# Kernel tuning notes

Hardware: AMD Instinct MI355X
Metric: run time of the kernel (lower is better)

## Reference

```python
import jax, jax.numpy as jnp
import numpy as np

B, C, H, W = 2, 192, 64, 64
HEADS, KS = 6, 7
HD = C // HEADS


def setup_inputs() -> dict:
    key = jax.random.key(0)
    ks = jax.random.split(key, 6)
    s = 0.02
    return {
        "x": jax.random.normal(ks[0], (B, C, H, W), jnp.float32),
        "W_qkv1": jax.random.normal(ks[1], (3 * C, C, 1, 1), jnp.float32) * s,
        "b_qkv1": jnp.zeros((3 * C,), jnp.float32),
        "W_qkv2": jax.random.normal(ks[2], (3 * C, 1, 3, 3), jnp.float32) * s,  # depthwise
        "b_qkv2": jnp.zeros((3 * C,), jnp.float32),
        "temperature": jnp.ones((HEADS, 1, 1, 1), jnp.float32),
        "rpb": jax.random.normal(ks[3], (HEADS, 2 * KS - 1, 2 * KS - 1), jnp.float32) * s,
        "W_proj": jax.random.normal(ks[4], (C, C, 1, 1), jnp.float32) * s,
        "b_proj": jnp.zeros((C,), jnp.float32),
    }


def _conv(x, w, b, pad, groups=1):
    y = jax.lax.conv_general_dilated(
        x, w, (1, 1), pad,
        dimension_numbers=("NCHW", "OIHW", "NCHW"),
        feature_group_count=groups)
    return y + b[None, :, None, None]


def _l2norm(t, eps=1e-12):
    n = jnp.sqrt(jnp.sum(t * t, axis=-1, keepdims=True))
    return t / jnp.maximum(n, eps)


def _nbr_idx(L, K):
    # NATTEN shifted-window neighborhood (dilation=1): window start clamped to image.
    start = jnp.clip(jnp.arange(L) - K // 2, 0, L - K)
    idx = start[:, None] + jnp.arange(K)[None, :]        # [L,K] absolute neighbor index
    rel = idx - jnp.arange(L)[:, None] + (K - 1)         # [L,K] rpb table index
    return idx, rel


def _forward(x, W_qkv1, b_qkv1, W_qkv2, b_qkv2, temperature, rpb, W_proj, b_proj):
    Bq, Cq, Hh, Ww = x.shape
    heads = rpb.shape[0]
    K = (rpb.shape[1] + 1) // 2
    hd = Cq // heads
    qkv = _conv(_conv(x, W_qkv1, b_qkv1, "VALID"), W_qkv2, b_qkv2, "SAME", groups=3 * Cq)
    qkv = qkv.reshape(Bq, 3, heads, hd, Hh, Ww).transpose(1, 0, 2, 4, 5, 3)  # [3,B,h,H,W,d]
    q, k, v = qkv[0], qkv[1], qkv[2]
    q = _l2norm(q)
    k = _l2norm(k)
    idx_i, rel_i = _nbr_idx(Hh, K)
    idx_j, rel_j = _nbr_idx(Ww, K)
    ii = idx_i[:, None, :, None]  # [H,1,K,1]
    jj = idx_j[None, :, None, :]  # [1,W,1,K] -> broadcast [H,W,K,K]
    k_nb = k[:, :, ii, jj, :]     # [B,h,H,W,K,K,d]
    attn = jnp.einsum("bhijd,bhijkld->bhijkl", q, k_nb)
    bias = rpb[:, rel_i[:, None, :, None], rel_j[None, :, None, :]]  # [h,H,W,K,K]
    attn = (attn + bias[None]) * temperature.reshape(1, heads, 1, 1, 1, 1)
    attn = jax.nn.softmax(attn.reshape(Bq, heads, Hh, Ww, K * K), axis=-1)
    v_nb = v[:, :, ii, jj, :].reshape(Bq, heads, Hh, Ww, K * K, hd)
    out = jnp.einsum("bhijk,bhijkd->bhijd", attn, v_nb)
    out = out.transpose(0, 1, 4, 2, 3).reshape(Bq, Cq, Hh, Ww)
    return _conv(out, W_proj, b_proj, "VALID")


def reference(x, W_qkv1, b_qkv1, W_qkv2, b_qkv2, temperature, rpb, W_proj, b_proj):
    return _forward(x, W_qkv1, b_qkv1, W_qkv2, b_qkv2, temperature, rpb, W_proj, b_proj)
```

## Files before the change

### kernel.cpp

```cpp
#include <hip/hip_runtime.h>
#include <math.h>

#define HW 4096

typedef __attribute__((ext_vector_type(8))) short short8;
typedef __attribute__((ext_vector_type(4))) float floatx4;

__device__ inline float bflo(unsigned u) { return __uint_as_float(u << 16); }
__device__ inline float bfhi(unsigned u) { return __uint_as_float(u & 0xffff0000u); }
__device__ inline unsigned short f2bf(float x) {
    unsigned u = __float_as_uint(x);
    return (unsigned short)((u + 0x7fffu + ((u >> 16) & 1u)) >> 16);
}
__device__ inline unsigned f2bf2(float lo, float hi) {
    unsigned a = __float_as_uint(lo), b = __float_as_uint(hi);
    a = (a + 0x7fffu + ((a >> 16) & 1u)) >> 16;
    b = (b + 0x7fffu + ((b >> 16) & 1u)) & 0xffff0000u;
    return a | b;
}
__device__ inline float qred(float x) {
    x += __int_as_float(__builtin_amdgcn_update_dpp(0, __float_as_int(x), 0xB1, 0xF, 0xF, true));
    x += __int_as_float(__builtin_amdgcn_update_dpp(0, __float_as_int(x), 0x4E, 0xF, 0xF, true));
    return x;
}


__global__ __launch_bounds__(256) void k_cvt(const float* __restrict__ W1,
    const float* __restrict__ Wp, unsigned short* __restrict__ Wb1,
    unsigned short* __restrict__ Wbp)
{
    int idx = blockIdx.x * 256 + threadIdx.x;
    if (idx < 110592) Wb1[idx] = f2bf(W1[idx]);
    else if (idx < 147456) Wbp[idx - 110592] = f2bf(Wp[idx - 110592]);
}

__global__ __launch_bounds__(256) void k_xt(const float* __restrict__ x,
    unsigned short* __restrict__ xT)
{
    __shared__ __align__(16) unsigned short tsm[64 * 196];
    const int t = threadIdx.x;
    const int px0 = blockIdx.x << 6;
    const int b = blockIdx.y;
    const float* xb = x + ((size_t)b * 192 << 12);
    #pragma unroll
    for (int pass = 0; pass < 12; ++pass) {
        int c = pass * 16 + (t >> 4);
        int p4 = t & 15;
        float4 v = *(const float4*)&xb[((size_t)c << 12) + px0 + p4 * 4];
        tsm[(p4 * 4 + 0) * 196 + c] = f2bf(v.x);
        tsm[(p4 * 4 + 1) * 196 + c] = f2bf(v.y);
        tsm[(p4 * 4 + 2) * 196 + c] = f2bf(v.z);
        tsm[(p4 * 4 + 3) * 196 + c] = f2bf(v.w);
    }
    __syncthreads();
    #pragma unroll
    for (int pass = 0; pass < 6; ++pass) {
        int idx = pass * 256 + t;
        int m = idx / 24, c8 = idx % 24;
        uint2 lo = *(const uint2*)&tsm[m * 196 + c8 * 8];
        uint2 hi = *(const uint2*)&tsm[m * 196 + c8 * 8 + 4];
        uint4 o = make_uint4(lo.x, lo.y, hi.x, hi.y);
        *(uint4*)&xT[((size_t)(b << 12) + px0 + m) * 192 + c8 * 8] = o;
    }
}

__global__ __launch_bounds__(256) void k_gq(const unsigned short* __restrict__ xT,
    const unsigned short* __restrict__ Wb1, const float* __restrict__ b1,
    unsigned short* __restrict__ qkv)
{
    __shared__ __align__(16) unsigned short As[64 * 200];
    __shared__ __align__(16) unsigned short Bs[64 * 200];
    const int t = threadIdx.x;
    const int m0 = blockIdx.x * 64;
    const int n0 = blockIdx.y * 64;
    #pragma unroll
    for (int pass = 0; pass < 6; ++pass) {
        int idx = pass * 256 + t;
        int m = idx / 24, c16 = idx % 24;
        *(uint4*)&As[m * 200 + c16 * 8] = *(const uint4*)&xT[(size_t)(m0 + m) * 192 + c16 * 8];
        *(uint4*)&Bs[m * 200 + c16 * 8] = *(const uint4*)&Wb1[(size_t)(n0 + m) * 192 + c16 * 8];
    }
    __syncthreads();
    const int w = t >> 6, lane = t & 63;
    const int lm = lane & 15, lq = lane >> 4;
    floatx4 acc[4] = {};
    #pragma unroll
    for (int ks = 0; ks < 6; ++ks) {
        short8 bf = *(const short8*)&Bs[(w * 16 + lm) * 200 + ks * 32 + lq * 8];
        #pragma unroll
        for (int mt = 0; mt < 4; ++mt) {
            short8 af = *(const short8*)&As[(mt * 16 + lm) * 200 + ks * 32 + lq * 8];
            acc[mt] = __builtin_amdgcn_mfma_f32_16x16x32_bf16(af, bf, acc[mt], 0, 0, 0);
        }
    }
    __syncthreads();
    const float bias = b1[n0 + w * 16 + lm];
    #pragma unroll
    for (int mt = 0; mt < 4; ++mt)
        #pragma unroll
        for (int r = 0; r < 4; ++r)
            As[(mt * 16 + lq * 4 + r) * 72 + w * 16 + lm] = f2bf(acc[mt][r] + bias);
    __syncthreads();
    #pragma unroll
    for (int pass = 0; pass < 2; ++pass) {
        int idx = pass * 256 + t;
        int m = idx >> 3, n8 = idx & 7;
        uint4 val = *(const uint4*)&As[m * 72 + n8 * 8];
        int mg = m0 + m;
        int b = mg >> 12, px = mg & 4095;
        int oc = n0 + n8 * 8;
        int g = oc >> 5, d = oc & 31;
        *(uint4*)&qkv[((((size_t)(b * 18 + g) << 12) + px) << 5) + d] = val;
    }
}

__global__ __launch_bounds__(256) void k_dw(const unsigned short* __restrict__ in,
    const float* __restrict__ W2, const float* __restrict__ b2,
    unsigned short* __restrict__ outq)
{
    __shared__ float wsm[288];
    __shared__ float bsm[32];
    const int t = threadIdx.x;
    const int bg = blockIdx.y;
    const int g = (bg >= 18) ? bg - 18 : bg;
    const int cbase = (g / 6) * 192 + (g % 6) * 32;
    for (int idx = t; idx < 288; idx += 256)
        wsm[idx] = W2[(cbase + (idx & 31)) * 9 + (idx >> 5)];
    if (t < 32) bsm[t] = b2[cbase + t];
    __syncthreads();
    const int px = (blockIdx.x << 6) + (t >> 2);
    const int d8 = t & 3;
    const int i = px >> 6, j = px & 63;
    const unsigned short* base = in + ((size_t)bg << 17);
    float acc[8];
    #pragma unroll
    for (int e = 0; e < 8; ++e) acc[e] = bsm[d8 * 8 + e];
    #pragma unroll
    for (int di = -1; di <= 1; ++di) {
        int ii = i + di;
        if (ii < 0 || ii > 63) continue;
        #pragma unroll
        for (int dj = -1; dj <= 1; ++dj) {
            int jj = j + dj;
            if (jj < 0 || jj > 63) continue;
            int tap = (di + 1) * 3 + dj + 1;
            uint4 u = *(const uint4*)(base + ((((ii << 6) + jj) << 5) + d8 * 8));
            const float* wt = &wsm[tap * 32 + d8 * 8];
            acc[0] = fmaf(bflo(u.x), wt[0], acc[0]);
            acc[1] = fmaf(bfhi(u.x), wt[1], acc[1]);
            acc[2] = fmaf(bflo(u.y), wt[2], acc[2]);
            acc[3] = fmaf(bfhi(u.y), wt[3], acc[3]);
            acc[4] = fmaf(bflo(u.z), wt[4], acc[4]);
            acc[5] = fmaf(bfhi(u.z), wt[5], acc[5]);
            acc[6] = fmaf(bflo(u.w), wt[6], acc[6]);
            acc[7] = fmaf(bfhi(u.w), wt[7], acc[7]);
        }
    }
    uint4 o;
    o.x = f2bf2(acc[0], acc[1]); o.y = f2bf2(acc[2], acc[3]);
    o.z = f2bf2(acc[4], acc[5]); o.w = f2bf2(acc[6], acc[7]);
    *(uint4*)(outq + ((size_t)bg << 17) + ((size_t)px << 5) + d8 * 8) = o;
}

__global__ __launch_bounds__(256) void k_attn(const unsigned short* __restrict__ qkv,
    const float* __restrict__ temp, const float* __restrict__ rpb,
    unsigned short* __restrict__ attnO)
{
    __shared__ __align__(16) unsigned kv[196 * 36];
    __shared__ float rpbs[169];
    const int t = threadIdx.x;
    const int ti = blockIdx.x >> 3, tj = blockIdx.x & 7;
    const int head = blockIdx.y, b = blockIdx.z;
    const int i0 = ti * 8, j0 = tj * 8;
    const int r0 = min(max(i0 - 3, 0), 50), c0 = min(max(j0 - 3, 0), 50);
    const unsigned short* kpl = qkv + ((size_t)(b * 18 + 6 + head) << 17);
    const unsigned short* vpl = qkv + ((size_t)(b * 18 + 12 + head) << 17);

    if (t < 196) {
        int r = (t * 2341) >> 15, cc = t - r * 14;
        int pix = ((r0 + r) << 6) + (c0 + cc);
        const unsigned* kg = (const unsigned*)(kpl + (pix << 5));
        const unsigned* vg = (const unsigned*)(vpl + (pix << 5));
        uint4 ku[4];
        float kf[32];
        float ss = 0.f;
        #pragma unroll
        for (int q = 0; q < 4; ++q) {
            ku[q] = *(const uint4*)(kg + q * 4);
            unsigned uu[4] = {ku[q].x, ku[q].y, ku[q].z, ku[q].w};
            #pragma unroll
            for (int e = 0; e < 4; ++e) {
                float lo = bflo(uu[e]), hi = bfhi(uu[e]);
                kf[q * 8 + e * 2] = lo; kf[q * 8 + e * 2 + 1] = hi;
                ss = fmaf(lo, lo, fmaf(hi, hi, ss));
            }
        }
        float rinv = 1.0f / fmaxf(sqrtf(ss), 1e-12f);
        #pragma unroll
        for (int q = 0; q < 4; ++q) {
            uint4 p;
            p.x = f2bf2(kf[q * 8 + 0] * rinv, kf[q * 8 + 1] * rinv);
            p.y = f2bf2(kf[q * 8 + 2] * rinv, kf[q * 8 + 3] * rinv);
            p.z = f2bf2(kf[q * 8 + 4] * rinv, kf[q * 8 + 5] * rinv);
            p.w = f2bf2(kf[q * 8 + 6] * rinv, kf[q * 8 + 7] * rinv);
            *(uint4*)&kv[t * 36 + q * 4] = p;
        }
        #pragma unroll
        for (int q = 0; q < 4; ++q)
            *(uint4*)&kv[t * 36 + 16 + q * 4] = *(const uint4*)(vg + q * 4);
    }
    if (t < 169) rpbs[t] = rpb[head * 169 + t];

    const int px = t >> 2, dsub = t & 3;
    const int li = px >> 3, lj = px & 7;
    const int i = i0 + li, j = j0 + lj;
    const unsigned short* qpl = qkv + ((size_t)(b * 18 + head) << 17);
    uint4 qu = *(const uint4*)(qpl + ((((i << 6) + j) << 5) + dsub * 8));
    float qf[8];
    qf[0] = bflo(qu.x); qf[1] = bfhi(qu.x);
    qf[2] = bflo(qu.y); qf[3] = bfhi(qu.y);
    qf[4] = bflo(qu.z); qf[5] = bfhi(qu.z);
    qf[6] = bflo(qu.w); qf[7] = bfhi(qu.w);
    float qs = 0.f;
    #pragma unroll
    for (int e = 0; e < 8; ++e) qs = fmaf(qf[e], qf[e], qs);
    qs = qred(qs);
    float qinv = 1.0f / fmaxf(sqrtf(qs), 1e-12f);
    #pragma unroll
    for (int e = 0; e < 8; ++e) qf[e] *= qinv;
    __syncthreads();

    const int si = min(max(i - 3, 0), 57), sj = min(max(j - 3, 0), 57);
    const int pr0 = si - r0, pc0 = sj - c0;
    const float th = temp[head];
    const int bi0 = (si - i + 6) * 13 + (sj - j + 6);
    const int nbase = pr0 * 14 + pc0;
    float a[49];
    #pragma unroll
    for (int ki = 0; ki < 7; ++ki) {
        #pragma unroll
        for (int kj = 0; kj < 7; ++kj) {
            int nb = nbase + ki * 14 + kj;
            uint4 uk = *(const uint4*)&kv[nb * 36 + dsub * 4];
            float dot;
            dot = qf[0] * bflo(uk.x);
            dot = fmaf(qf[1], bfhi(uk.x), dot);
            dot = fmaf(qf[2], bflo(uk.y), dot);
            dot = fmaf(qf[3], bfhi(uk.y), dot);
            dot = fmaf(qf[4], bflo(uk.z), dot);
            dot = fmaf(qf[5], bfhi(uk.z), dot);
            dot = fmaf(qf[6], bflo(uk.w), dot);
            dot = fmaf(qf[7], bfhi(uk.w), dot);
            dot = qred(dot);
            a[ki * 7 + kj] = (dot + rpbs[bi0 + ki * 13 + kj]) * th;
        }
    }

    float m = a[0];
    #pragma unroll
    for (int kk = 1; kk < 49; ++kk) m = fmaxf(m, a[kk]);
    float ssum = 0.f;
    #pragma unroll
    for (int kk = 0; kk < 49; ++kk) { a[kk] = __expf(a[kk] - m); ssum += a[kk]; }
    const float rs = 1.0f / ssum;

    float o[8];
    #pragma unroll
    for (int e = 0; e < 8; ++e) o[e] = 0.f;
    #pragma unroll
    for (int ki = 0; ki < 7; ++ki) {
        #pragma unroll
        for (int kj = 0; kj < 7; ++kj) {
            int nb = nbase + ki * 14 + kj;
            uint4 uv = *(const uint4*)&kv[nb * 36 + 16 + dsub * 4];
            float wgt = a[ki * 7 + kj];
            o[0] = fmaf(wgt, bflo(uv.x), o[0]);
            o[1] = fmaf(wgt, bfhi(uv.x), o[1]);
            o[2] = fmaf(wgt, bflo(uv.y), o[2]);
            o[3] = fmaf(wgt, bfhi(uv.y), o[3]);
            o[4] = fmaf(wgt, bflo(uv.z), o[4]);
            o[5] = fmaf(wgt, bfhi(uv.z), o[5]);
            o[6] = fmaf(wgt, bflo(uv.w), o[6]);
            o[7] = fmaf(wgt, bfhi(uv.w), o[7]);
        }
    }
    uint4 ov;
    ov.x = f2bf2(o[0] * rs, o[1] * rs);
    ov.y = f2bf2(o[2] * rs, o[3] * rs);
    ov.z = f2bf2(o[4] * rs, o[5] * rs);
    ov.w = f2bf2(o[6] * rs, o[7] * rs);
    *(uint4*)&attnO[((size_t)((b << 12) + (i << 6) + j)) * 192 + head * 32 + dsub * 8] = ov;
}

__global__ __launch_bounds__(256) void k_gp(const unsigned short* __restrict__ Ain,
    const unsigned short* __restrict__ Wbp, const float* __restrict__ bp,
    float* __restrict__ out)
{
    __shared__ __align__(16) unsigned short As[64 * 200];
    __shared__ __align__(16) unsigned short Bs[64 * 200];
    const int t = threadIdx.x;
    const int m0 = blockIdx.x * 64;
    const int n0 = blockIdx.y * 64;
    #pragma unroll
    for (int pass = 0; pass < 6; ++pass) {
        int idx = pass * 256 + t;
        int m = idx / 24, c16 = idx % 24;
        *(uint4*)&As[m * 200 + c16 * 8] = *(const uint4*)&Ain[(size_t)(m0 + m) * 192 + c16 * 8];
        *(uint4*)&Bs[m * 200 + c16 * 8] = *(const uint4*)&Wbp[(size_t)(n0 + m) * 192 + c16 * 8];
    }
    __syncthreads();
    const int w = t >> 6, lane = t & 63;
    const int lm = lane & 15, lq = lane >> 4;
    floatx4 acc[4] = {};
    #pragma unroll
    for (int ks = 0; ks < 6; ++ks) {
        short8 bf = *(const short8*)&Bs[(w * 16 + lm) * 200 + ks * 32 + lq * 8];
        #pragma unroll
        for (int mt = 0; mt < 4; ++mt) {
            short8 af = *(const short8*)&As[(mt * 16 + lm) * 200 + ks * 32 + lq * 8];
            acc[mt] = __builtin_amdgcn_mfma_f32_16x16x32_bf16(af, bf, acc[mt], 0, 0, 0);
        }
    }
    __syncthreads();
    float* fs = (float*)As;
    const float bias = bp[n0 + w * 16 + lm];
    #pragma unroll
    for (int mt = 0; mt < 4; ++mt)
        #pragma unroll
        for (int r = 0; r < 4; ++r)
            fs[(w * 16 + lm) * 68 + mt * 16 + lq * 4 + r] = acc[mt][r] + bias;
    __syncthreads();
    const int b = m0 >> 12, px0 = m0 & 4095;
    #pragma unroll
    for (int pass = 0; pass < 4; ++pass) {
        int idx = pass * 256 + t;
        int n = idx >> 4, m4 = idx & 15;
        float4 val = *(const float4*)&fs[n * 68 + m4 * 4];
        *(float4*)&out[((size_t)(b * 192 + n0 + n) << 12) + px0 + m4 * 4] = val;
    }
}

extern "C" void kernel_launch(void* const* d_in, const int* in_sizes, int n_in,
                              void* d_out, int out_size, void* d_ws, size_t ws_size,
                              hipStream_t stream) {
    const float* x    = (const float*)d_in[0];
    const float* W1   = (const float*)d_in[1];
    const float* b1   = (const float*)d_in[2];
    const float* W2   = (const float*)d_in[3];
    const float* b2   = (const float*)d_in[4];
    const float* temp = (const float*)d_in[5];
    const float* rpb  = (const float*)d_in[6];
    const float* Wp   = (const float*)d_in[7];
    const float* bp   = (const float*)d_in[8];
    float* out = (float*)d_out;

    char* ws = (char*)d_ws;
    unsigned short* Wb1   = (unsigned short*)(ws);
    unsigned short* Wbp   = (unsigned short*)(ws + 221184);
    unsigned short* xT    = (unsigned short*)(ws + 294912);
    unsigned short* qkv1b = (unsigned short*)(ws + 3440640);
    unsigned short* qkv2b = (unsigned short*)(ws + 12877824);
    unsigned short* attnO = (unsigned short*)(ws + 22315008);

    k_cvt <<<dim3(576), 256, 0, stream>>>(W1, Wp, Wb1, Wbp);
    k_xt  <<<dim3(64, 2), 256, 0, stream>>>(x, xT);
    k_gq  <<<dim3(128, 9), 256, 0, stream>>>(xT, Wb1, b1, qkv1b);
    k_dw  <<<dim3(64, 36), 256, 0, stream>>>(qkv1b, W2, b2, qkv2b);
    k_attn<<<dim3(64, 6, 2), 256, 0, stream>>>(qkv2b, temp, rpb, attnO);
    k_gp  <<<dim3(128, 3), 256, 0, stream>>>(attnO, Wbp, bp, out);
}
```

Before: 117.2 us.

## Use MFMA for neighborhood attention over full 14x14 halo and retile transpose

The attention kernel now computes QK^T with bf16 MFMA against all 196 halo keys of the 8x8 tile, then masks out-of-window entries before the softmax. Probabilities are written to LDS as fp16 and multiplied by a transposed fp16 V tile using f16 MFMA. This replaces the scalar per-neighbor dot products and DPP reductions, at the cost of about four times more raw FLOPs and extra LDS traffic. Separately, the input transpose kernel is split across channel blocks, giving it more blocks and a padded float LDS tile.

```diff
diff --git a/kernel.cpp b/kernel.cpp
--- a/kernel.cpp
+++ b/kernel.cpp
@@ -4,6 +4,7 @@
 #define HW 4096
 
 typedef __attribute__((ext_vector_type(8))) short short8;
+typedef __attribute__((ext_vector_type(8))) _Float16 half8;
 typedef __attribute__((ext_vector_type(4))) float floatx4;
 
 __device__ inline float bflo(unsigned u) { return __uint_as_float(u << 16); }
@@ -18,10 +19,9 @@
     b = (b + 0x7fffu + ((b >> 16) & 1u)) & 0xffff0000u;
     return a | b;
 }
-__device__ inline float qred(float x) {
-    x += __int_as_float(__builtin_amdgcn_update_dpp(0, __float_as_int(x), 0xB1, 0xF, 0xF, true));
-    x += __int_as_float(__builtin_amdgcn_update_dpp(0, __float_as_int(x), 0x4E, 0xF, 0xF, true));
-    return x;
+__device__ inline unsigned short f2h(float x) {
+    _Float16 h = (_Float16)x;
+    return __builtin_bit_cast(unsigned short, h);
 }
 
 
@@ -37,30 +37,26 @@
 __global__ __launch_bounds__(256) void k_xt(const float* __restrict__ x,
     unsigned short* __restrict__ xT)
 {
-    __shared__ __align__(16) unsigned short tsm[64 * 196];
+    __shared__ float smf[64 * 65];
     const int t = threadIdx.x;
     const int px0 = blockIdx.x << 6;
-    const int b = blockIdx.y;
-    const float* xb = x + ((size_t)b * 192 << 12);
-    #pragma unroll
-    for (int pass = 0; pass < 12; ++pass) {
-        int c = pass * 16 + (t >> 4);
-        int p4 = t & 15;
-        float4 v = *(const float4*)&xb[((size_t)c << 12) + px0 + p4 * 4];
-        tsm[(p4 * 4 + 0) * 196 + c] = f2bf(v.x);
-        tsm[(p4 * 4 + 1) * 196 + c] = f2bf(v.y);
-        tsm[(p4 * 4 + 2) * 196 + c] = f2bf(v.z);
-        tsm[(p4 * 4 + 3) * 196 + c] = f2bf(v.w);
-    }
-    __syncthreads();
-    #pragma unroll
-    for (int pass = 0; pass < 6; ++pass) {
-        int idx = pass * 256 + t;
-        int m = idx / 24, c8 = idx % 24;
-        uint2 lo = *(const uint2*)&tsm[m * 196 + c8 * 8];
-        uint2 hi = *(const uint2*)&tsm[m * 196 + c8 * 8 + 4];
-        uint4 o = make_uint4(lo.x, lo.y, hi.x, hi.y);
-        *(uint4*)&xT[((size_t)(b << 12) + px0 + m) * 192 + c8 * 8] = o;
+    const int c0 = blockIdx.y << 6;
+    const int b = blockIdx.z;
+    const float* xb = x + ((size_t)(b * 192 + c0) << 12) + px0;
+    const int pxl = t & 63, csub = t >> 6;
+    #pragma unroll
+    for (int pass = 0; pass < 16; ++pass) {
+        int c = pass * 4 + csub;
+        smf[pxl * 65 + c] = xb[((size_t)c << 12) + pxl];
+    }
+    __syncthreads();
+    const int c2 = t & 31, psub = t >> 5;
+    unsigned* ob = (unsigned*)xT;
+    #pragma unroll
+    for (int pass = 0; pass < 8; ++pass) {
+        int px = pass * 8 + psub;
+        unsigned v = f2bf2(smf[px * 65 + c2 * 2], smf[px * 65 + c2 * 2 + 1]);
+        ob[((size_t)((b << 12) + px0 + px)) * 96 + (c0 >> 1) + c2] = v;
     }
 }
 
@@ -166,28 +162,32 @@
     const float* __restrict__ temp, const float* __restrict__ rpb,
     unsigned short* __restrict__ attnO)
 {
-    __shared__ __align__(16) unsigned kv[196 * 36];
-    __shared__ float rpbs[169];
+    __shared__ __align__(16) char lds[45224];
+    unsigned short* Ks  = (unsigned short*)lds;
+    unsigned short* Ps  = (unsigned short*)lds;
+    unsigned short* Vts = (unsigned short*)(lds + 29696);
+    float* rpbs = (float*)(lds + 44544);
+
     const int t = threadIdx.x;
     const int ti = blockIdx.x >> 3, tj = blockIdx.x & 7;
     const int head = blockIdx.y, b = blockIdx.z;
     const int i0 = ti * 8, j0 = tj * 8;
     const int r0 = min(max(i0 - 3, 0), 50), c0 = min(max(j0 - 3, 0), 50);
+    const unsigned short* qpl = qkv + ((size_t)(b * 18 + head) << 17);
     const unsigned short* kpl = qkv + ((size_t)(b * 18 + 6 + head) << 17);
     const unsigned short* vpl = qkv + ((size_t)(b * 18 + 12 + head) << 17);
 
     if (t < 196) {
         int r = (t * 2341) >> 15, cc = t - r * 14;
         int pix = ((r0 + r) << 6) + (c0 + cc);
-        const unsigned* kg = (const unsigned*)(kpl + (pix << 5));
-        const unsigned* vg = (const unsigned*)(vpl + (pix << 5));
-        uint4 ku[4];
+        const uint4* kg = (const uint4*)(kpl + (pix << 5));
+        const uint4* vg = (const uint4*)(vpl + (pix << 5));
         float kf[32];
         float ss = 0.f;
         #pragma unroll
         for (int q = 0; q < 4; ++q) {
-            ku[q] = *(const uint4*)(kg + q * 4);
-            unsigned uu[4] = {ku[q].x, ku[q].y, ku[q].z, ku[q].w};
+            uint4 ku = kg[q];
+            unsigned uu[4] = {ku.x, ku.y, ku.z, ku.w};
             #pragma unroll
             for (int e = 0; e < 4; ++e) {
                 float lo = bflo(uu[e]), hi = bfhi(uu[e]);
@@ -203,19 +203,31 @@
             p.y = f2bf2(kf[q * 8 + 2] * rinv, kf[q * 8 + 3] * rinv);
             p.z = f2bf2(kf[q * 8 + 4] * rinv, kf[q * 8 + 5] * rinv);
             p.w = f2bf2(kf[q * 8 + 6] * rinv, kf[q * 8 + 7] * rinv);
-            *(uint4*)&kv[t * 36 + q * 4] = p;
-        }
-        #pragma unroll
-        for (int q = 0; q < 4; ++q)
-            *(uint4*)&kv[t * 36 + 16 + q * 4] = *(const uint4*)(vg + q * 4);
+            *(uint4*)&Ks[t * 40 + q * 8] = p;
+        }
+        #pragma unroll
+        for (int q = 0; q < 4; ++q) {
+            uint4 vu = vg[q];
+            unsigned uu[4] = {vu.x, vu.y, vu.z, vu.w};
+            #pragma unroll
+            for (int e = 0; e < 4; ++e) {
+                Vts[(q * 8 + e * 2) * 232 + t]     = f2h(bflo(uu[e]));
+                Vts[(q * 8 + e * 2 + 1) * 232 + t] = f2h(bfhi(uu[e]));
+            }
+        }
+    }
+    for (int idx = t; idx < 448; idx += 256) {
+        int row = (idx * 2341) >> 15;
+        int c = idx - row * 14;
+        ((unsigned*)(Vts + row * 232))[98 + c] = 0u;
     }
     if (t < 169) rpbs[t] = rpb[head * 169 + t];
 
-    const int px = t >> 2, dsub = t & 3;
-    const int li = px >> 3, lj = px & 7;
-    const int i = i0 + li, j = j0 + lj;
-    const unsigned short* qpl = qkv + ((size_t)(b * 18 + head) << 17);
-    uint4 qu = *(const uint4*)(qpl + ((((i << 6) + j) << 5) + dsub * 8));
+    const int w = t >> 6, lane = t & 63;
+    const int lm = lane & 15, lq = lane >> 4;
+    const int px = w * 16 + lm;
+    const int i = i0 + (px >> 3), j = j0 + (px & 7);
+    uint4 qu = *(const uint4*)(qpl + ((((i << 6) + j) << 5) + lq * 8));
     float qf[8];
     qf[0] = bflo(qu.x); qf[1] = bfhi(qu.x);
     qf[2] = bflo(qu.y); qf[3] = bfhi(qu.y);
@@ -224,72 +236,92 @@
     float qs = 0.f;
     #pragma unroll
     for (int e = 0; e < 8; ++e) qs = fmaf(qf[e], qf[e], qs);
-    qs = qred(qs);
+    qs += __shfl_xor(qs, 16);
+    qs += __shfl_xor(qs, 32);
     float qinv = 1.0f / fmaxf(sqrtf(qs), 1e-12f);
-    #pragma unroll
-    for (int e = 0; e < 8; ++e) qf[e] *= qinv;
+    short8 bq;
+    #pragma unroll
+    for (int e = 0; e < 8; ++e) bq[e] = (short)f2bf(qf[e] * qinv);
+    __syncthreads();
+
+    floatx4 acc[13];
+    #pragma unroll
+    for (int mt = 0; mt < 13; ++mt) {
+        short8 ak = *(const short8*)&Ks[(mt * 16 + lm) * 40 + lq * 8];
+        floatx4 z = {0.f, 0.f, 0.f, 0.f};
+        acc[mt] = __builtin_amdgcn_mfma_f32_16x16x32_bf16(ak, bq, z, 0, 0, 0);
+    }
     __syncthreads();
 
     const int si = min(max(i - 3, 0), 57), sj = min(max(j - 3, 0), 57);
-    const int pr0 = si - r0, pc0 = sj - c0;
+    const int vloi = si - r0, vloj = sj - c0;
+    const int oi = r0 - i + 6, oj = c0 - j + 6;
     const float th = temp[head];
-    const int bi0 = (si - i + 6) * 13 + (sj - j + 6);
-    const int nbase = pr0 * 14 + pc0;
-    float a[49];
-    #pragma unroll
-    for (int ki = 0; ki < 7; ++ki) {
-        #pragma unroll
-        for (int kj = 0; kj < 7; ++kj) {
-            int nb = nbase + ki * 14 + kj;
-            uint4 uk = *(const uint4*)&kv[nb * 36 + dsub * 4];
-            float dot;
-            dot = qf[0] * bflo(uk.x);
-            dot = fmaf(qf[1], bfhi(uk.x), dot);
-            dot = fmaf(qf[2], bflo(uk.y), dot);
-            dot = fmaf(qf[3], bfhi(uk.y), dot);
-            dot = fmaf(qf[4], bflo(uk.z), dot);
-            dot = fmaf(qf[5], bfhi(uk.z), dot);
-            dot = fmaf(qf[6], bflo(uk.w), dot);
-            dot = fmaf(qf[7], bfhi(uk.w), dot);
-            dot = qred(dot);
-            a[ki * 7 + kj] = (dot + rpbs[bi0 + ki * 13 + kj]) * th;
-        }
-    }
-
-    float m = a[0];
-    #pragma unroll
-    for (int kk = 1; kk < 49; ++kk) m = fmaxf(m, a[kk]);
+    float mx = -1e30f;
+    #pragma unroll
+    for (int mt = 0; mt < 13; ++mt) {
+        int nb0 = mt * 16 + lq * 4;
+        int rh0 = (nb0 * 2341) >> 15;
+        int ch0 = nb0 - rh0 * 14;
+        #pragma unroll
+        for (int r = 0; r < 4; ++r) {
+            int ch = ch0 + r, rh = rh0;
+            if (ch >= 14) { ch -= 14; rh += 1; }
+            int bidx = (rh + oi) * 13 + (ch + oj);
+            float bias = rpbs[max(0, min(168, bidx))];
+            bool valid = ((unsigned)(rh - vloi) <= 6u) && ((unsigned)(ch - vloj) <= 6u);
+            float s = (acc[mt][r] + bias) * th;
+            s = valid ? s : -1e30f;
+            acc[mt][r] = s;
+            mx = fmaxf(mx, s);
+        }
+    }
+    mx = fmaxf(mx, __shfl_xor(mx, 16));
+    mx = fmaxf(mx, __shfl_xor(mx, 32));
     float ssum = 0.f;
     #pragma unroll
-    for (int kk = 0; kk < 49; ++kk) { a[kk] = __expf(a[kk] - m); ssum += a[kk]; }
+    for (int mt = 0; mt < 13; ++mt)
+        #pragma unroll
+        for (int r = 0; r < 4; ++r) {
+            float e = __expf(acc[mt][r] - mx);
+            acc[mt][r] = e;
+            ssum += e;
+        }
+    ssum += __shfl_xor(ssum, 16);
+    ssum += __shfl_xor(ssum, 32);
     const float rs = 1.0f / ssum;
 
-    float o[8];
-    #pragma unroll
-    for (int e = 0; e < 8; ++e) o[e] = 0.f;
-    #pragma unroll
-    for (int ki = 0; ki < 7; ++ki) {
-        #pragma unroll
-        for (int kj = 0; kj < 7; ++kj) {
-            int nb = nbase + ki * 14 + kj;
-            uint4 uv = *(const uint4*)&kv[nb * 36 + 16 + dsub * 4];
-            float wgt = a[ki * 7 + kj];
-            o[0] = fmaf(wgt, bflo(uv.x), o[0]);
-            o[1] = fmaf(wgt, bfhi(uv.x), o[1]);
-            o[2] = fmaf(wgt, bflo(uv.y), o[2]);
-            o[3] = fmaf(wgt, bfhi(uv.y), o[3]);
-            o[4] = fmaf(wgt, bflo(uv.z), o[4]);
-            o[5] = fmaf(wgt, bfhi(uv.z), o[5]);
-            o[6] = fmaf(wgt, bflo(uv.w), o[6]);
-            o[7] = fmaf(wgt, bfhi(uv.w), o[7]);
-        }
-    }
-    uint4 ov;
-    ov.x = f2bf2(o[0] * rs, o[1] * rs);
-    ov.y = f2bf2(o[2] * rs, o[3] * rs);
-    ov.z = f2bf2(o[4] * rs, o[5] * rs);
-    ov.w = f2bf2(o[6] * rs, o[7] * rs);
-    *(uint4*)&attnO[((size_t)((b << 12) + (i << 6) + j)) * 192 + head * 32 + dsub * 8] = ov;
+    if (lane < 32) {
+        uint4 z4 = {0u, 0u, 0u, 0u};
+        *(uint4*)&Ps[(w * 16 + (lane >> 1)) * 232 + 208 + (lane & 1) * 8] = z4;
+    }
+    #pragma unroll
+    for (int mt = 0; mt < 13; ++mt) {
+        unsigned lo = (unsigned)f2h(acc[mt][0] * rs) | ((unsigned)f2h(acc[mt][1] * rs) << 16);
+        unsigned hi = (unsigned)f2h(acc[mt][2] * rs) | ((unsigned)f2h(acc[mt][3] * rs) << 16);
+        *(uint2*)&Ps[px * 232 + mt * 16 + lq * 4] = make_uint2(lo, hi);
+    }
+    __syncthreads();
+
+    floatx4 oacc[2] = {};
+    #pragma unroll
+    for (int ks = 0; ks < 7; ++ks) {
+        half8 ap = *(const half8*)&Ps[(w * 16 + lm) * 232 + ks * 32 + lq * 8];
+        #pragma unroll
+        for (int n2 = 0; n2 < 2; ++n2) {
+            half8 bv = *(const half8*)&Vts[(n2 * 16 + lm) * 232 + ks * 32 + lq * 8];
+            oacc[n2] = __builtin_amdgcn_mfma_f32_16x16x32_f16(ap, bv, oacc[n2], 0, 0, 0);
+        }
+    }
+    #pragma unroll
+    for (int n2 = 0; n2 < 2; ++n2)
+        #pragma unroll
+        for (int r = 0; r < 4; ++r) {
+            int p2 = w * 16 + lq * 4 + r;
+            int i2 = i0 + (p2 >> 3), j2 = j0 + (p2 & 7);
+            attnO[((size_t)((b << 12) + (i2 << 6) + j2)) * 192 + head * 32 + n2 * 16 + lm]
+                = f2bf(oacc[n2][r]);
+        }
 }
 
 __global__ __launch_bounds__(256) void k_gp(const unsigned short* __restrict__ Ain,
@@ -363,7 +395,7 @@
     unsigned short* attnO = (unsigned short*)(ws + 22315008);
 
     k_cvt <<<dim3(576), 256, 0, stream>>>(W1, Wp, Wb1, Wbp);
-    k_xt  <<<dim3(64, 2), 256, 0, stream>>>(x, xT);
+    k_xt  <<<dim3(64, 3, 2), 256, 0, stream>>>(x, xT);
     k_gq  <<<dim3(128, 9), 256, 0, stream>>>(xT, Wb1, b1, qkv1b);
     k_dw  <<<dim3(64, 36), 256, 0, stream>>>(qkv1b, W2, b2, qkv2b);
     k_attn<<<dim3(64, 6, 2), 256, 0, stream>>>(qkv2b, temp, rpb, attnO);
```

Result: faster. 114.8 us (-2.0%).
